# Kernel optimization log

Hardware: AMD Instinct MI355X
Metric: run time of the kernel (lower is better)

## Reference

```python
import jax, jax.numpy as jnp
import numpy as np

B, S, D = 4, 4096, 768  # batch, seq_len, n_units
NEG = -1000000000.0      # masked_fill value from the torch source


def setup_inputs() -> dict:
    key = jax.random.key(0)
    ks = jax.random.split(key, 12)
    scale = 1.0 / np.sqrt(D)
    inp = {
        "query": jax.random.normal(ks[0], (B, S, D), jnp.float32),
        "key_": jax.random.normal(ks[1], (B, S, D), jnp.float32),
        "value": jax.random.normal(ks[2], (B, S, D), jnp.float32),
        # nn.Linear weights are [out, in]; forward computes x @ W.T + b
        "Wq": jax.random.normal(ks[3], (D, D), jnp.float32) * scale,
        "bq": jnp.zeros((D,), jnp.float32),
        "Wk": jax.random.normal(ks[4], (D, D), jnp.float32) * scale,
        "bk": jnp.zeros((D,), jnp.float32),
        "Wv": jax.random.normal(ks[5], (D, D), jnp.float32) * scale,
        "bv": jnp.zeros((D,), jnp.float32),
        "Wo": jax.random.normal(ks[6], (D, D), jnp.float32) * scale,
        "bo": jnp.zeros((D,), jnp.float32),
        # broadcastable causal mask [1, S, S]; 0 -> masked
        "mask": jnp.tril(jnp.ones((S, S), jnp.int32))[None, :, :],
    }
    return inp


def reference(query, key_, value, Wq, bq, Wk, bk, Wv, bv, Wo, bo, mask):
    # QKV projections (torch Linear: x @ W.T + b)
    q = jnp.einsum("bsd,ed->bse", query, Wq) + bq
    k = jnp.einsum("bsd,ed->bse", key_, Wk) + bk
    v = jnp.einsum("bsd,ed->bse", value, Wv) + bv
    # scores: NOTE source scales by n_units**0.5 (full model dim, no head split)
    weights = jnp.einsum("bqd,bkd->bqk", q, k) / jnp.sqrt(jnp.float32(D))
    weights = jnp.where(mask == 0, jnp.float32(NEG), weights)
    weights = jax.nn.softmax(weights, axis=-1)
    # dropout is identity in eval/deterministic reference
    attended = jnp.einsum("bqk,bkd->bqd", weights, v)
    return jnp.einsum("bsd,ed->bse", attended, Wo) + bo
```

## Files before the change

kernel.cpp:

```cpp
#include <hip/hip_runtime.h>
#include <hip/hip_bf16.h>
#include <stdint.h>

#define DI __device__ __forceinline__

typedef __bf16 bf16x4 __attribute__((ext_vector_type(4)));
typedef __bf16 bf16x8 __attribute__((ext_vector_type(8)));
typedef float  f32x4  __attribute__((ext_vector_type(4)));

static constexpr int  BATCH = 4;
static constexpr int  SEQ   = 4096;
static constexpr int  DIM   = 768;
static constexpr long TOK   = (long)BATCH * SEQ;
static constexpr int  QT    = SEQ / 128;
static constexpr int  NTRI  = QT * (QT + 1) / 2;
static constexpr float SCALE = 0.0360843918243516150f;

__global__ void cvt3_kernel(const float* __restrict__ a, const float* __restrict__ b,
                            const float* __restrict__ c, __bf16* __restrict__ oa,
                            __bf16* __restrict__ ob, __bf16* __restrict__ oc, long n4){
  const float* in  = blockIdx.y == 0 ? a : blockIdx.y == 1 ? b : c;
  __bf16*      out = blockIdx.y == 0 ? oa : blockIdx.y == 1 ? ob : oc;
  long i = (long)blockIdx.x * blockDim.x + threadIdx.x;
  const long stride = (long)gridDim.x * blockDim.x;
  for(; i < n4; i += stride){
    float4 v = ((const float4*)in)[i];
    bf16x4 o = { (__bf16)v.x, (__bf16)v.y, (__bf16)v.z, (__bf16)v.w };
    ((bf16x4*)out)[i] = o;
  }
}
__global__ void cvt4_kernel(const float* __restrict__ a, const float* __restrict__ b,
                            const float* __restrict__ c, const float* __restrict__ d,
                            __bf16* __restrict__ oa, __bf16* __restrict__ ob,
                            __bf16* __restrict__ oc, __bf16* __restrict__ od, long n4){
  const float* in  = blockIdx.y == 0 ? a : blockIdx.y == 1 ? b : blockIdx.y == 2 ? c : d;
  __bf16*      out = blockIdx.y == 0 ? oa : blockIdx.y == 1 ? ob : blockIdx.y == 2 ? oc : od;
  long i = (long)blockIdx.x * blockDim.x + threadIdx.x;
  const long stride = (long)gridDim.x * blockDim.x;
  for(; i < n4; i += stride){
    float4 v = ((const float4*)in)[i];
    bf16x4 o = { (__bf16)v.x, (__bf16)v.y, (__bf16)v.z, (__bf16)v.w };
    ((bf16x4*)out)[i] = o;
  }
}

DI int swz_off(int r, int c){ return (r << 7) + ((c ^ (r & 7)) << 4); }

template<int NT, int R>
DI void stage(const __bf16* __restrict__ src, long ld, char* lds, int tid){
  const int w = tid >> 6, l = tid & 63;
  const int rsub = l >> 3;
  const int kc   = (l & 7) ^ rsub;
  const __bf16* g = src + (long)(w * 8 + rsub) * ld + kc * 8;
  char* d = lds + (w << 10);
  constexpr int RPC = (NT / 64) * 8;
  #pragma unroll
  for(int i = 0; i < R / RPC; ++i){
    __builtin_amdgcn_global_load_lds(
        (const __attribute__((address_space(1))) void*)(g + (long)(i * RPC) * ld),
        (__attribute__((address_space(3))) void*)(d + i * RPC * 128), 16, 0, 0);
  }
}

DI bf16x8 frag_ld(const char* lds, int row, int c){
  return *(const bf16x8*)(lds + swz_off(row, c));
}

DI void mma_tile(const char* As, const char* Bs, int lane, int wr, int wc, f32x4 acc[4][4]){
  #pragma unroll
  for(int kk = 0; kk < 2; ++kk){
    const int c = kk * 4 + (lane >> 4);
    bf16x8 a[4], b[4];
    #pragma unroll
    for(int i = 0; i < 4; ++i) a[i] = frag_ld(As, wr + i * 16 + (lane & 15), c);
    #pragma unroll
    for(int j = 0; j < 4; ++j) b[j] = frag_ld(Bs, wc + j * 16 + (lane & 15), c);
    #pragma unroll
    for(int i = 0; i < 4; ++i)
      #pragma unroll
      for(int j = 0; j < 4; ++j)
        acc[i][j] = __builtin_amdgcn_mfma_f32_16x16x32_bf16(a[i], b[j], acc[i][j], 0, 0, 0);
  }
}

template<bool OUTF32, bool BIASM>
__global__ __launch_bounds__(512)
void gemm256_bt(const __bf16* __restrict__ A, const __bf16* __restrict__ B,
                const float* __restrict__ bias, void* __restrict__ C,
                int K, long lda, long ldb, long ldc){
  __shared__ __attribute__((aligned(128))) char As[16384];
  __shared__ __attribute__((aligned(128))) char Bs[32768];
  const int tid = threadIdx.x, lane = tid & 63, w = tid >> 6;
  const int wr = (w >> 2) * 64, wc = (w & 3) * 64;
  const long m0 = (long)blockIdx.y * 128, n0 = (long)blockIdx.x * 256;
  f32x4 acc[4][4] = {};
  for(int k0 = 0; k0 < K; k0 += 64){
    stage<512, 128>(A + m0 * lda + k0, lda, As, tid);
    stage<512, 256>(B + n0 * ldb + k0, ldb, Bs, tid);
    __syncthreads();
    mma_tile(As, Bs, lane, wr, wc, acc);
    __syncthreads();
  }
  const int cl = lane & 15, rq = (lane >> 4) * 4;
  #pragma unroll
  for(int i = 0; i < 4; ++i)
    #pragma unroll
    for(int j = 0; j < 4; ++j){
      const long gc = n0 + wc + j * 16 + cl;
      #pragma unroll
      for(int e = 0; e < 4; ++e){
        const long gr = m0 + wr + i * 16 + rq + e;
        float v = acc[i][j][e] + (BIASM ? bias[gr] : bias[gc]);
        if(OUTF32) ((float*)C)[gr * ldc + gc] = v;
        else       ((__bf16*)C)[gr * ldc + gc] = (__bf16)v;
      }
    }
}

__global__ __launch_bounds__(512)
void qk_kernel(const __bf16* __restrict__ qb, const __bf16* __restrict__ kb,
               __bf16* __restrict__ Pc){
  const int b = blockIdx.y;
  const int t2 = blockIdx.x;
  int Qi = (int)((sqrtf(4.0f * t2 + 1.0f) - 1.0f) * 0.5f);
  while((Qi + 1) * (Qi + 2) <= t2) Qi++;
  while(Qi * (Qi + 1) > t2) Qi--;
  const int ki = t2 - Qi * (Qi + 1);
  const __bf16* Aq = qb + ((long)b * SEQ + Qi * 256) * DIM;
  const __bf16* Bk = kb + ((long)b * SEQ + ki * 128) * DIM;
  __shared__ __attribute__((aligned(128))) char As[32768];
  __shared__ __attribute__((aligned(128))) char Bs[16384];
  const int tid = threadIdx.x, lane = tid & 63, w = tid >> 6;
  const int wr = (w >> 1) * 64, wc = (w & 1) * 64;
  f32x4 acc[4][4] = {};
  for(int k0 = 0; k0 < DIM; k0 += 64){
    stage<512, 256>(Aq + k0, DIM, As, tid);
    stage<512, 128>(Bk + k0, DIM, Bs, tid);
    __syncthreads();
    mma_tile(As, Bs, lane, wr, wc, acc);
    __syncthreads();
  }
  const int cl = lane & 15, rq = (lane >> 4) * 4;
  #pragma unroll
  for(int i = 0; i < 4; ++i){
    const int rbase = wr + i * 16;
    const int qi = 2 * Qi + (rbase >> 7);
    if(ki > qi) continue;
    const bool diag = (ki == qi);
    __bf16* tile = Pc + ((long)b * NTRI + (long)qi * (qi + 1) / 2 + ki) * 16384;
    #pragma unroll
    for(int j = 0; j < 4; ++j){
      const int c = wc + j * 16 + cl;
      #pragma unroll
      for(int e = 0; e < 4; ++e){
        const int rloc = (rbase + rq + e) & 127;
        float p = (diag && c > rloc) ? 0.0f
                  : __expf(fminf(acc[i][j][e] * SCALE, 30.0f));
        tile[rloc * 128 + c] = (__bf16)p;
      }
    }
  }
}

__global__ void rowsum(const __bf16* __restrict__ Pc, float* __restrict__ rlrow){
  const int gr = blockIdx.x * 4 + (threadIdx.x >> 6);
  const int lane = threadIdx.x & 63;
  const int b = gr >> 12, r = gr & 4095;
  const int qi = r >> 7, rloc = r & 127;
  const __bf16* base = Pc + ((long)b * NTRI + (long)qi * (qi + 1) / 2) * 16384
                       + rloc * 128;
  float s = 0.f;
  for(int ki = 0; ki <= qi; ++ki){
    uint32_t u = *(const uint32_t*)(base + (long)ki * 16384 + lane * 2);
    s += __uint_as_float(u << 16) + __uint_as_float(u & 0xffff0000u);
  }
  #pragma unroll
  for(int off = 32; off; off >>= 1) s += __shfl_xor(s, off);
  if(lane == 0) rlrow[gr] = 1.0f / s;
}

__global__ __launch_bounds__(512)
void pv_kernel(const __bf16* __restrict__ Pc, const float* __restrict__ rlrow,
               const __bf16* __restrict__ vbT, __bf16* __restrict__ att){
  const int b = blockIdx.z, qi = 31 - blockIdx.y;
  const long n0 = (long)blockIdx.x * 256;
  __shared__ __attribute__((aligned(128))) char As[16384];
  __shared__ __attribute__((aligned(128))) char Bs[32768];
  __shared__ float sRl[128];
  const int tid = threadIdx.x, lane = tid & 63, w = tid >> 6;
  const int wr = (w >> 2) * 64, wc = (w & 3) * 64;
  if(tid < 128) sRl[tid] = rlrow[b * SEQ + qi * 128 + tid];
  f32x4 acc[4][4] = {};
  const __bf16* Pq = Pc + ((long)b * NTRI + (long)qi * (qi + 1) / 2) * 16384;
  const __bf16* Bv = vbT + n0 * TOK + (long)b * SEQ;
  __syncthreads();
  for(int kt = 0; kt <= qi; ++kt){
    #pragma unroll
    for(int half = 0; half < 2; ++half){
      stage<512, 128>(Pq + (long)kt * 16384 + half * 64, 128, As, tid);
      stage<512, 256>(Bv + (long)kt * 128 + half * 64, TOK, Bs, tid);
      __syncthreads();
      mma_tile(As, Bs, lane, wr, wc, acc);
      __syncthreads();
    }
  }
  const int cl = lane & 15, rq = (lane >> 4) * 4;
  #pragma unroll
  for(int i = 0; i < 4; ++i)
    #pragma unroll
    for(int j = 0; j < 4; ++j){
      const long gc = n0 + wc + j * 16 + cl;
      #pragma unroll
      for(int e = 0; e < 4; ++e){
        const int rloc = wr + i * 16 + rq + e;
        float v = acc[i][j][e] * sRl[rloc];
        att[((long)b * SEQ + qi * 128 + rloc) * DIM + gc] = (__bf16)v;
      }
    }
}

extern "C" void kernel_launch(void* const* d_in, const int* in_sizes, int n_in,
                              void* d_out, int out_size, void* d_ws, size_t ws_size,
                              hipStream_t stream){
  const float* query = (const float*)d_in[0];
  const float* key_  = (const float*)d_in[1];
  const float* value = (const float*)d_in[2];
  const float* Wq = (const float*)d_in[3];
  const float* bq = (const float*)d_in[4];
  const float* Wk = (const float*)d_in[5];
  const float* bk = (const float*)d_in[6];
  const float* Wv = (const float*)d_in[7];
  const float* bv = (const float*)d_in[8];
  const float* Wo = (const float*)d_in[9];
  const float* bo = (const float*)d_in[10];

  char* p = (char*)d_ws;
  auto carve = [&](size_t bytes)->char*{
    char* r = p; p += (bytes + 255) & ~(size_t)255; return r;
  };
  const size_t tb = (size_t)TOK * DIM * 2;
  __bf16* xq  = (__bf16*)carve(tb);
  __bf16* xk  = (__bf16*)carve(tb);
  __bf16* xv  = (__bf16*)carve(tb);
  __bf16* qb  = (__bf16*)carve(tb);
  __bf16* kb  = (__bf16*)carve(tb);
  __bf16* vbT = (__bf16*)carve(tb);
  __bf16* Wqb = (__bf16*)carve((size_t)DIM * DIM * 2);
  __bf16* Wkb = (__bf16*)carve((size_t)DIM * DIM * 2);
  __bf16* Wvb = (__bf16*)carve((size_t)DIM * DIM * 2);
  __bf16* Wob = (__bf16*)carve((size_t)DIM * DIM * 2);
  __bf16* Pc  = (__bf16*)carve((size_t)BATCH * NTRI * 16384 * 2);
  float*  rlr = (float*)carve((size_t)TOK * 4);
  __bf16* att = xq;
  if((size_t)(p - (char*)d_ws) > ws_size) return;

  const long nIn4 = TOK * DIM / 4, nW4 = (long)DIM * DIM / 4;
  dim3 g3(2048, 3), g4((unsigned)((nW4 + 255) / 256), 4);
  cvt3_kernel<<<g3, 256, 0, stream>>>(query, key_, value, xq, xk, xv, nIn4);
  cvt4_kernel<<<g4, 256, 0, stream>>>(Wq, Wk, Wv, Wo, Wqb, Wkb, Wvb, Wob, nW4);

  dim3 gProj(DIM / 256, TOK / 128);
  gemm256_bt<false, false><<<gProj, 512, 0, stream>>>(xq, Wqb, bq, qb, DIM, DIM, DIM, DIM);
  gemm256_bt<false, false><<<gProj, 512, 0, stream>>>(xk, Wkb, bk, kb, DIM, DIM, DIM, DIM);
  dim3 gVT(TOK / 256, DIM / 128);
  gemm256_bt<false, true><<<gVT, 512, 0, stream>>>(Wvb, xv, bv, vbT, DIM, DIM, DIM, TOK);

  dim3 gQK(272, BATCH);
  qk_kernel<<<gQK, 512, 0, stream>>>(qb, kb, Pc);

  rowsum<<<TOK / 4, 256, 0, stream>>>(Pc, rlr);

  dim3 gPV(DIM / 256, QT, BATCH);
  pv_kernel<<<gPV, 512, 0, stream>>>(Pc, rlr, vbT, att);

  gemm256_bt<true, false><<<gProj, 512, 0, stream>>>(att, Wob, bo, d_out, DIM, DIM, DIM, DIM);
}
```

Baseline: 329.1 us.

## Fuse input bf16 conversion into projections and row sums into QK kernel

Drops the separate fp32-to-bf16 conversion of query/key/value: the projection GEMMs now load fp32 rows and convert them while writing LDS, and the Q and K projections share one launch. The rowsum pass is removed; the QK kernel builds per-row exp sums with shuffles and atomicAdd into a zeroed buffer, and the PV kernel takes the reciprocal. This removes a full read/write of the activations and a re-read of the probability matrix. In exchange, the fp32 stage uses ordinary loads instead of direct global-to-LDS loads, and atomics add contention and nondeterministic summation order.

```diff
diff --git a/kernel.cpp b/kernel.cpp
--- a/kernel.cpp
+++ b/kernel.cpp
@@ -16,19 +16,6 @@
 static constexpr int  NTRI  = QT * (QT + 1) / 2;
 static constexpr float SCALE = 0.0360843918243516150f;
 
-__global__ void cvt3_kernel(const float* __restrict__ a, const float* __restrict__ b,
-                            const float* __restrict__ c, __bf16* __restrict__ oa,
-                            __bf16* __restrict__ ob, __bf16* __restrict__ oc, long n4){
-  const float* in  = blockIdx.y == 0 ? a : blockIdx.y == 1 ? b : c;
-  __bf16*      out = blockIdx.y == 0 ? oa : blockIdx.y == 1 ? ob : oc;
-  long i = (long)blockIdx.x * blockDim.x + threadIdx.x;
-  const long stride = (long)gridDim.x * blockDim.x;
-  for(; i < n4; i += stride){
-    float4 v = ((const float4*)in)[i];
-    bf16x4 o = { (__bf16)v.x, (__bf16)v.y, (__bf16)v.z, (__bf16)v.w };
-    ((bf16x4*)out)[i] = o;
-  }
-}
 __global__ void cvt4_kernel(const float* __restrict__ a, const float* __restrict__ b,
                             const float* __restrict__ c, const float* __restrict__ d,
                             __bf16* __restrict__ oa, __bf16* __restrict__ ob,
@@ -46,19 +33,35 @@
 
 DI int swz_off(int r, int c){ return (r << 7) + ((c ^ (r & 7)) << 4); }
 
-template<int NT, int R>
+template<int R>
 DI void stage(const __bf16* __restrict__ src, long ld, char* lds, int tid){
   const int w = tid >> 6, l = tid & 63;
   const int rsub = l >> 3;
   const int kc   = (l & 7) ^ rsub;
   const __bf16* g = src + (long)(w * 8 + rsub) * ld + kc * 8;
   char* d = lds + (w << 10);
-  constexpr int RPC = (NT / 64) * 8;
-  #pragma unroll
-  for(int i = 0; i < R / RPC; ++i){
+  #pragma unroll
+  for(int i = 0; i < R / 64; ++i){
     __builtin_amdgcn_global_load_lds(
-        (const __attribute__((address_space(1))) void*)(g + (long)(i * RPC) * ld),
-        (__attribute__((address_space(3))) void*)(d + i * RPC * 128), 16, 0, 0);
+        (const __attribute__((address_space(1))) void*)(g + (long)(i * 64) * ld),
+        (__attribute__((address_space(3))) void*)(d + i * 8192), 16, 0, 0);
+  }
+}
+
+template<int R>
+DI void stage_cvt(const float* __restrict__ src, long ld, char* lds, int tid){
+  const int w = tid >> 6, l = tid & 63;
+  const int rsub = l >> 3;
+  const int kc   = (l & 7) ^ rsub;
+  const float* g = src + (long)(w * 8 + rsub) * ld + kc * 8;
+  char* d = lds + (w << 10) + ((l & 63) << 4);
+  #pragma unroll
+  for(int i = 0; i < R / 64; ++i){
+    const float4* s = (const float4*)(g + (long)(i * 64) * ld);
+    float4 v0 = s[0], v1 = s[1];
+    bf16x8 o = { (__bf16)v0.x, (__bf16)v0.y, (__bf16)v0.z, (__bf16)v0.w,
+                 (__bf16)v1.x, (__bf16)v1.y, (__bf16)v1.z, (__bf16)v1.w };
+    *(bf16x8*)(d + i * 8192) = o;
   }
 }
 
@@ -83,20 +86,41 @@
   }
 }
 
-template<bool OUTF32, bool BIASM>
-__global__ __launch_bounds__(512)
-void gemm256_bt(const __bf16* __restrict__ A, const __bf16* __restrict__ B,
-                const float* __restrict__ bias, void* __restrict__ C,
-                int K, long lda, long ldb, long ldc){
+template<class FA, class FB>
+DI void kloop2(FA fa, long lda, FB fb, long ldb, int nt, int tid,
+               char* As, char* Bs, f32x4 acc[4][4]){
+  const int lane = tid & 63, w = tid >> 6;
+  const int wr = (w >> 2) * 64, wc = (w & 3) * 64;
+  for(int t = 0; t < nt; ++t){
+    stage<128>(fa(t), lda, As, tid);
+    stage<256>(fb(t), ldb, Bs, tid);
+    __syncthreads();
+    mma_tile(As, Bs, lane, wr, wc, acc);
+    __syncthreads();
+  }
+}
+
+__global__ __launch_bounds__(512)
+void proj_qk(const float* __restrict__ query, const float* __restrict__ key_,
+             const __bf16* __restrict__ Wqb, const __bf16* __restrict__ Wkb,
+             const float* __restrict__ bq, const float* __restrict__ bk,
+             __bf16* __restrict__ qb, __bf16* __restrict__ kb){
   __shared__ __attribute__((aligned(128))) char As[16384];
   __shared__ __attribute__((aligned(128))) char Bs[32768];
-  const int tid = threadIdx.x, lane = tid & 63, w = tid >> 6;
-  const int wr = (w >> 2) * 64, wc = (w & 3) * 64;
-  const long m0 = (long)blockIdx.y * 128, n0 = (long)blockIdx.x * 256;
-  f32x4 acc[4][4] = {};
-  for(int k0 = 0; k0 < K; k0 += 64){
-    stage<512, 128>(A + m0 * lda + k0, lda, As, tid);
-    stage<512, 256>(B + n0 * ldb + k0, ldb, Bs, tid);
+  const int z = blockIdx.y, bid = blockIdx.x, tid = threadIdx.x;
+  const float*  X = z ? key_ : query;
+  const __bf16* W = z ? Wkb : Wqb;
+  const float*  bias = z ? bk : bq;
+  __bf16*       C = z ? kb : qb;
+  const long m0 = (long)(bid / 3) * 128, n0 = (bid % 3) * 256;
+  const float*  Ar = X + m0 * DIM;
+  const __bf16* Br = W + n0 * DIM;
+  f32x4 acc[4][4] = {};
+  const int lane = tid & 63, w = tid >> 6;
+  const int wr = (w >> 2) * 64, wc = (w & 3) * 64;
+  for(int t = 0; t < DIM / 64; ++t){
+    stage_cvt<128>(Ar + t * 64, DIM, As, tid);
+    stage<256>(Br + t * 64, DIM, Bs, tid);
     __syncthreads();
     mma_tile(As, Bs, lane, wr, wc, acc);
     __syncthreads();
@@ -110,18 +134,48 @@
       #pragma unroll
       for(int e = 0; e < 4; ++e){
         const long gr = m0 + wr + i * 16 + rq + e;
-        float v = acc[i][j][e] + (BIASM ? bias[gr] : bias[gc]);
-        if(OUTF32) ((float*)C)[gr * ldc + gc] = v;
-        else       ((__bf16*)C)[gr * ldc + gc] = (__bf16)v;
+        C[gr * DIM + gc] = (__bf16)(acc[i][j][e] + bias[gc]);
+      }
+    }
+}
+
+__global__ __launch_bounds__(512)
+void proj_vT(const __bf16* __restrict__ Wvb, const float* __restrict__ value,
+             const float* __restrict__ bv, __bf16* __restrict__ vbT){
+  __shared__ __attribute__((aligned(128))) char As[16384];
+  __shared__ __attribute__((aligned(128))) char Bs[32768];
+  const int bid = blockIdx.x, tid = threadIdx.x;
+  const long m0 = (long)(bid / 64) * 128, n0 = (long)(bid % 64) * 256;
+  const __bf16* Ar = Wvb + m0 * DIM;
+  const float*  Br = value + n0 * DIM;
+  f32x4 acc[4][4] = {};
+  const int lane = tid & 63, w = tid >> 6;
+  const int wr = (w >> 2) * 64, wc = (w & 3) * 64;
+  for(int t = 0; t < DIM / 64; ++t){
+    stage<128>(Ar + t * 64, DIM, As, tid);
+    stage_cvt<256>(Br + t * 64, DIM, Bs, tid);
+    __syncthreads();
+    mma_tile(As, Bs, lane, wr, wc, acc);
+    __syncthreads();
+  }
+  const int cl = lane & 15, rq = (lane >> 4) * 4;
+  #pragma unroll
+  for(int i = 0; i < 4; ++i)
+    #pragma unroll
+    for(int j = 0; j < 4; ++j){
+      const long gc = n0 + wc + j * 16 + cl;
+      #pragma unroll
+      for(int e = 0; e < 4; ++e){
+        const long gr = m0 + wr + i * 16 + rq + e;
+        vbT[gr * TOK + gc] = (__bf16)(acc[i][j][e] + bv[gr]);
       }
     }
 }
 
 __global__ __launch_bounds__(512)
 void qk_kernel(const __bf16* __restrict__ qb, const __bf16* __restrict__ kb,
-               __bf16* __restrict__ Pc){
-  const int b = blockIdx.y;
-  const int t2 = blockIdx.x;
+               __bf16* __restrict__ Pc, float* __restrict__ rlsum){
+  const int b = blockIdx.y, t2 = blockIdx.x, tid = threadIdx.x;
   int Qi = (int)((sqrtf(4.0f * t2 + 1.0f) - 1.0f) * 0.5f);
   while((Qi + 1) * (Qi + 2) <= t2) Qi++;
   while(Qi * (Qi + 1) > t2) Qi--;
@@ -130,12 +184,12 @@
   const __bf16* Bk = kb + ((long)b * SEQ + ki * 128) * DIM;
   __shared__ __attribute__((aligned(128))) char As[32768];
   __shared__ __attribute__((aligned(128))) char Bs[16384];
-  const int tid = threadIdx.x, lane = tid & 63, w = tid >> 6;
+  const int lane = tid & 63, w = tid >> 6;
   const int wr = (w >> 1) * 64, wc = (w & 1) * 64;
   f32x4 acc[4][4] = {};
-  for(int k0 = 0; k0 < DIM; k0 += 64){
-    stage<512, 256>(Aq + k0, DIM, As, tid);
-    stage<512, 128>(Bk + k0, DIM, Bs, tid);
+  for(int t = 0; t < DIM / 64; ++t){
+    stage<256>(Aq + t * 64, DIM, As, tid);
+    stage<128>(Bk + t * 64, DIM, Bs, tid);
     __syncthreads();
     mma_tile(As, Bs, lane, wr, wc, acc);
     __syncthreads();
@@ -148,6 +202,7 @@
     if(ki > qi) continue;
     const bool diag = (ki == qi);
     __bf16* tile = Pc + ((long)b * NTRI + (long)qi * (qi + 1) / 2 + ki) * 16384;
+    float rsum[4] = {0.f, 0.f, 0.f, 0.f};
     #pragma unroll
     for(int j = 0; j < 4; ++j){
       const int c = wc + j * 16 + cl;
@@ -157,53 +212,40 @@
         float p = (diag && c > rloc) ? 0.0f
                   : __expf(fminf(acc[i][j][e] * SCALE, 30.0f));
         tile[rloc * 128 + c] = (__bf16)p;
-      }
-    }
-  }
-}
-
-__global__ void rowsum(const __bf16* __restrict__ Pc, float* __restrict__ rlrow){
-  const int gr = blockIdx.x * 4 + (threadIdx.x >> 6);
-  const int lane = threadIdx.x & 63;
-  const int b = gr >> 12, r = gr & 4095;
-  const int qi = r >> 7, rloc = r & 127;
-  const __bf16* base = Pc + ((long)b * NTRI + (long)qi * (qi + 1) / 2) * 16384
-                       + rloc * 128;
-  float s = 0.f;
-  for(int ki = 0; ki <= qi; ++ki){
-    uint32_t u = *(const uint32_t*)(base + (long)ki * 16384 + lane * 2);
-    s += __uint_as_float(u << 16) + __uint_as_float(u & 0xffff0000u);
-  }
-  #pragma unroll
-  for(int off = 32; off; off >>= 1) s += __shfl_xor(s, off);
-  if(lane == 0) rlrow[gr] = 1.0f / s;
-}
-
-__global__ __launch_bounds__(512)
-void pv_kernel(const __bf16* __restrict__ Pc, const float* __restrict__ rlrow,
+        rsum[e] += p;
+      }
+    }
+    #pragma unroll
+    for(int e = 0; e < 4; ++e){
+      float s = rsum[e];
+      s += __shfl_xor(s, 1); s += __shfl_xor(s, 2);
+      s += __shfl_xor(s, 4); s += __shfl_xor(s, 8);
+      if(cl == 0){
+        const long gr = (long)b * SEQ + Qi * 256 + rbase + rq + e;
+        atomicAdd(&rlsum[gr], s);
+      }
+    }
+  }
+}
+
+__global__ __launch_bounds__(512)
+void pv_kernel(const __bf16* __restrict__ Pc, const float* __restrict__ rlsum,
                const __bf16* __restrict__ vbT, __bf16* __restrict__ att){
-  const int b = blockIdx.z, qi = 31 - blockIdx.y;
-  const long n0 = (long)blockIdx.x * 256;
   __shared__ __attribute__((aligned(128))) char As[16384];
   __shared__ __attribute__((aligned(128))) char Bs[32768];
   __shared__ float sRl[128];
-  const int tid = threadIdx.x, lane = tid & 63, w = tid >> 6;
-  const int wr = (w >> 2) * 64, wc = (w & 3) * 64;
-  if(tid < 128) sRl[tid] = rlrow[b * SEQ + qi * 128 + tid];
-  f32x4 acc[4][4] = {};
+  const int b = blockIdx.z, qi = 31 - blockIdx.y, tid = threadIdx.x;
+  const long n0 = (long)blockIdx.x * 256;
+  if(tid < 128) sRl[tid] = 1.0f / rlsum[b * SEQ + qi * 128 + tid];
   const __bf16* Pq = Pc + ((long)b * NTRI + (long)qi * (qi + 1) / 2) * 16384;
   const __bf16* Bv = vbT + n0 * TOK + (long)b * SEQ;
-  __syncthreads();
-  for(int kt = 0; kt <= qi; ++kt){
-    #pragma unroll
-    for(int half = 0; half < 2; ++half){
-      stage<512, 128>(Pq + (long)kt * 16384 + half * 64, 128, As, tid);
-      stage<512, 256>(Bv + (long)kt * 128 + half * 64, TOK, Bs, tid);
-      __syncthreads();
-      mma_tile(As, Bs, lane, wr, wc, acc);
-      __syncthreads();
-    }
-  }
+  f32x4 acc[4][4] = {};
+  auto fa = [&](int t){ return Pq + (long)(t >> 1) * 16384 + (t & 1) * 64; };
+  auto fb = [&](int t){ return Bv + t * 64; };
+  kloop2(fa, 128, fb, TOK, 2 * (qi + 1), tid, As, Bs, acc);
+
+  const int lane = tid & 63, w = tid >> 6;
+  const int wr = (w >> 2) * 64, wc = (w & 3) * 64;
   const int cl = lane & 15, rq = (lane >> 4) * 4;
   #pragma unroll
   for(int i = 0; i < 4; ++i)
@@ -215,6 +257,35 @@
         const int rloc = wr + i * 16 + rq + e;
         float v = acc[i][j][e] * sRl[rloc];
         att[((long)b * SEQ + qi * 128 + rloc) * DIM + gc] = (__bf16)v;
+      }
+    }
+}
+
+__global__ __launch_bounds__(512)
+void oproj(const __bf16* __restrict__ att, const __bf16* __restrict__ Wob,
+           const float* __restrict__ bo, float* __restrict__ out){
+  __shared__ __attribute__((aligned(128))) char As[16384];
+  __shared__ __attribute__((aligned(128))) char Bs[32768];
+  const int bid = blockIdx.x, tid = threadIdx.x;
+  const long n0 = (bid % 3) * 256, m0 = (long)(bid / 3) * 128;
+  const __bf16* Ar = att + m0 * DIM;
+  const __bf16* Br = Wob + n0 * DIM;
+  f32x4 acc[4][4] = {};
+  auto fa = [&](int t){ return Ar + t * 64; };
+  auto fb = [&](int t){ return Br + t * 64; };
+  kloop2(fa, DIM, fb, DIM, DIM / 64, tid, As, Bs, acc);
+  const int lane = tid & 63, w = tid >> 6;
+  const int wr = (w >> 2) * 64, wc = (w & 3) * 64;
+  const int cl = lane & 15, rq = (lane >> 4) * 4;
+  #pragma unroll
+  for(int i = 0; i < 4; ++i)
+    #pragma unroll
+    for(int j = 0; j < 4; ++j){
+      const long gc = n0 + wc + j * 16 + cl;
+      #pragma unroll
+      for(int e = 0; e < 4; ++e){
+        const long gr = m0 + wr + i * 16 + rq + e;
+        out[gr * DIM + gc] = acc[i][j][e] + bo[gc];
       }
     }
 }
@@ -239,39 +310,29 @@
     char* r = p; p += (bytes + 255) & ~(size_t)255; return r;
   };
   const size_t tb = (size_t)TOK * DIM * 2;
-  __bf16* xq  = (__bf16*)carve(tb);
-  __bf16* xk  = (__bf16*)carve(tb);
-  __bf16* xv  = (__bf16*)carve(tb);
   __bf16* qb  = (__bf16*)carve(tb);
   __bf16* kb  = (__bf16*)carve(tb);
   __bf16* vbT = (__bf16*)carve(tb);
+  __bf16* att = (__bf16*)carve(tb);
   __bf16* Wqb = (__bf16*)carve((size_t)DIM * DIM * 2);
   __bf16* Wkb = (__bf16*)carve((size_t)DIM * DIM * 2);
   __bf16* Wvb = (__bf16*)carve((size_t)DIM * DIM * 2);
   __bf16* Wob = (__bf16*)carve((size_t)DIM * DIM * 2);
   __bf16* Pc  = (__bf16*)carve((size_t)BATCH * NTRI * 16384 * 2);
   float*  rlr = (float*)carve((size_t)TOK * 4);
-  __bf16* att = xq;
   if((size_t)(p - (char*)d_ws) > ws_size) return;
 
-  const long nIn4 = TOK * DIM / 4, nW4 = (long)DIM * DIM / 4;
-  dim3 g3(2048, 3), g4((unsigned)((nW4 + 255) / 256), 4);
-  cvt3_kernel<<<g3, 256, 0, stream>>>(query, key_, value, xq, xk, xv, nIn4);
+  const long nW4 = (long)DIM * DIM / 4;
+  dim3 g4((unsigned)((nW4 + 255) / 256), 4);
+  hipMemsetAsync(rlr, 0, (size_t)TOK * 4, stream);
   cvt4_kernel<<<g4, 256, 0, stream>>>(Wq, Wk, Wv, Wo, Wqb, Wkb, Wvb, Wob, nW4);
 
-  dim3 gProj(DIM / 256, TOK / 128);
-  gemm256_bt<false, false><<<gProj, 512, 0, stream>>>(xq, Wqb, bq, qb, DIM, DIM, DIM, DIM);
-  gemm256_bt<false, false><<<gProj, 512, 0, stream>>>(xk, Wkb, bk, kb, DIM, DIM, DIM, DIM);
-  dim3 gVT(TOK / 256, DIM / 128);
-  gemm256_bt<false, true><<<gVT, 512, 0, stream>>>(Wvb, xv, bv, vbT, DIM, DIM, DIM, TOK);
-
-  dim3 gQK(272, BATCH);
-  qk_kernel<<<gQK, 512, 0, stream>>>(qb, kb, Pc);
-
-  rowsum<<<TOK / 4, 256, 0, stream>>>(Pc, rlr);
-
-  dim3 gPV(DIM / 256, QT, BATCH);
-  pv_kernel<<<gPV, 512, 0, stream>>>(Pc, rlr, vbT, att);
-
-  gemm256_bt<true, false><<<gProj, 512, 0, stream>>>(att, Wob, bo, d_out, DIM, DIM, DIM, DIM);
-}
+  proj_qk<<<dim3(384, 2), 512, 0, stream>>>(query, key_, Wqb, Wkb, bq, bk, qb, kb);
+  proj_vT<<<384, 512, 0, stream>>>(Wvb, value, bv, vbT);
+
+  qk_kernel<<<dim3(272, BATCH), 512, 0, stream>>>(qb, kb, Pc, rlr);
+
+  pv_kernel<<<dim3(3, QT, BATCH), 512, 0, stream>>>(Pc, rlr, vbT, att);
+
+  oproj<<<384, 512, 0, stream>>>(att, Wob, bo, (float*)d_out);
+}
```

New measurement: 321.1 us. 1.02x faster.
